# Performance work log

Hardware: AMD Instinct MI355X
Metric: run time of the kernel (lower is better)

## Reference

```python
import jax, jax.numpy as jnp
import numpy as np

DIM = 384
HEADS = 6
HIDDEN = int(DIM * 4.0)
EPS = 1e-6

def setup_inputs() -> dict:
    key = jax.random.key(0)
    ks = jax.random.split(key, 8)
    s = 0.02
    return {
        "x": jax.random.normal(ks[0], (4, 2048, DIM), dtype=jnp.float32),
        "w_qkv": jax.random.normal(ks[1], (DIM, 3 * DIM), dtype=jnp.float32) * s,
        "b_qkv": jnp.zeros((3 * DIM,), dtype=jnp.float32),
        "w_proj": jax.random.normal(ks[2], (DIM, DIM), dtype=jnp.float32) * s,
        "b_proj": jnp.zeros((DIM,), dtype=jnp.float32),
        "w_fc1": jax.random.normal(ks[3], (DIM, HIDDEN), dtype=jnp.float32) * s,
        "b_fc1": jnp.zeros((HIDDEN,), dtype=jnp.float32),
        "w_fc2": jax.random.normal(ks[4], (HIDDEN, DIM), dtype=jnp.float32) * s,
        "b_fc2": jnp.zeros((DIM,), dtype=jnp.float32),
        "g1": jnp.ones((DIM,), dtype=jnp.float32),
        "beta1": jnp.zeros((DIM,), dtype=jnp.float32),
        "g2": jnp.ones((DIM,), dtype=jnp.float32),
        "beta2": jnp.zeros((DIM,), dtype=jnp.float32),
    }

def _layernorm(x, g, b):
    mu = jnp.mean(x, axis=-1, keepdims=True)
    var = jnp.mean(jnp.square(x - mu), axis=-1, keepdims=True)
    return (x - mu) * jax.lax.rsqrt(var + EPS) * g + b

def _attention(x, w_qkv, b_qkv, w_proj, b_proj):
    B, N, C = x.shape
    H = HEADS
    Dh = C // H
    qkv = x @ w_qkv + b_qkv                      # [B,N,3C]
    qkv = qkv.reshape(B, N, 3, H, Dh)
    q = jnp.transpose(qkv[:, :, 0], (0, 2, 1, 3))  # [B,H,N,Dh]
    k = jnp.transpose(qkv[:, :, 1], (0, 2, 1, 3))
    v = jnp.transpose(qkv[:, :, 2], (0, 2, 1, 3))
    scale = Dh ** -0.5
    attn = jnp.einsum('bhnd,bhmd->bhnm', q, k) * scale
    attn = jax.nn.softmax(attn, axis=-1)
    out = jnp.einsum('bhnm,bhmd->bhnd', attn, v)
    out = jnp.transpose(out, (0, 2, 1, 3)).reshape(B, N, C)
    return out @ w_proj + b_proj

def _mlp(x, w_fc1, b_fc1, w_fc2, b_fc2):
    h = jax.nn.gelu(x @ w_fc1 + b_fc1, approximate=False)
    return h @ w_fc2 + b_fc2

def reference(x, w_qkv, b_qkv, w_proj, b_proj, w_fc1, b_fc1, w_fc2, b_fc2, g1, beta1, g2, beta2):
    x = x + _attention(_layernorm(x, g1, beta1), w_qkv, b_qkv, w_proj, b_proj)
    x = x + _mlp(_layernorm(x, g2, beta2), w_fc1, b_fc1, w_fc2, b_fc2)
    return x
```

## Files before the change

kernel.cpp:

```cpp
#include <hip/hip_runtime.h>
#include <hip/hip_bf16.h>

#define TOK 8192
#define CDIM 384
#define HEADS 6
#define DH 64
#define HID 1536
#define SEQ 2048

typedef short bf16x8 __attribute__((ext_vector_type(8)));
typedef float f32x4 __attribute__((ext_vector_type(4)));
typedef void __attribute__((address_space(1))) GV;
typedef void __attribute__((address_space(3))) SV;

__device__ __forceinline__ short f2bf(float f) {
    __hip_bfloat16 h = __float2bfloat16(f);
    return *reinterpret_cast<short*>(&h);
}

__device__ __forceinline__ int pack_bf2(float a, float b) {
    __hip_bfloat162 h2 = __float22bfloat162_rn(make_float2(a, b));
    int r;
    __builtin_memcpy(&r, &h2, 4);
    return r;
}

__device__ __forceinline__ void gl_lds16(const short* g, short* lds) {
    __builtin_amdgcn_global_load_lds((GV*)g, (SV*)lds, 16, 0, 0);
}

__device__ __forceinline__ float gelu_exact(float v) {
    return 0.5f * v * (1.0f + erff(v * 0.70710678118654752f));
}

#define SWZ4(r) ((((r) & 3) ^ (((r) >> 2) & 3)))

__global__ __launch_bounds__(128) void ln_kernel(const float* __restrict__ x,
                                                 const float* __restrict__ g,
                                                 const float* __restrict__ bta,
                                                 short* __restrict__ y) {
    const int row = blockIdx.x;
    const float* xr = x + (size_t)row * CDIM;
    const int t = threadIdx.x;
    float v0 = xr[t], v1 = xr[t + 128], v2 = xr[t + 256];
    float s = v0 + v1 + v2;
    float ss = v0 * v0 + v1 * v1 + v2 * v2;
#pragma unroll
    for (int off = 1; off < 64; off <<= 1) {
        s += __shfl_xor(s, off);
        ss += __shfl_xor(ss, off);
    }
    __shared__ float sh[4];
    const int wv = t >> 6;
    if ((t & 63) == 0) { sh[wv] = s; sh[2 + wv] = ss; }
    __syncthreads();
    s = sh[0] + sh[1];
    ss = sh[2] + sh[3];
    const float mu = s * (1.0f / CDIM);
    const float var = ss * (1.0f / CDIM) - mu * mu;
    const float rs = rsqrtf(var + 1e-6f);
    short* yr = y + (size_t)row * CDIM;
    yr[t]       = f2bf((v0 - mu) * rs * g[t]       + bta[t]);
    yr[t + 128] = f2bf((v1 - mu) * rs * g[t + 128] + bta[t + 128]);
    yr[t + 256] = f2bf((v2 - mu) * rs * g[t + 256] + bta[t + 256]);
}

__global__ __launch_bounds__(256) void transpose_bf16(const float* __restrict__ w,
                                                      short* __restrict__ wT,
                                                      int K, int N) {
    __shared__ float t[32][33];
    const int bx = blockIdx.x * 32, by = blockIdx.y * 32;
    const int tx = threadIdx.x & 31, ty = threadIdx.x >> 5;
#pragma unroll
    for (int i = 0; i < 4; ++i)
        t[ty + i * 8][tx] = w[(size_t)(by + ty + i * 8) * N + bx + tx];
    __syncthreads();
#pragma unroll
    for (int i = 0; i < 4; ++i)
        wT[(size_t)(bx + ty + i * 8) * K + by + tx] = f2bf(t[tx][ty + i * 8]);
}

template <int MODE, int MT>
__global__ __launch_bounds__(256) void mfma_gemm(const short* __restrict__ A,
                                                 const short* __restrict__ WT,
                                                 const float* __restrict__ bias,
                                                 const float* __restrict__ resid,
                                                 float* __restrict__ outF,
                                                 short* __restrict__ outB,
                                                 short* __restrict__ qb,
                                                 short* __restrict__ kb,
                                                 short* __restrict__ vtb,
                                                 int M, int N, int K) {
    constexpr int BN = (MT == 4) ? 128 : 64;
    __shared__ __align__(16) short As[128 * 32];
    __shared__ __align__(16) short Bs[BN * 32];

    const int tid  = threadIdx.x;
    const int w    = tid >> 6;
    const int lane = tid & 63;
    const int quad = lane >> 4;
    const int n15  = lane & 15;
    const int wr   = (MT == 4) ? (w >> 1) : w;
    const int wc   = (MT == 4) ? (w & 1) : 0;
    const int m0   = blockIdx.y * 128;
    const int n0   = blockIdx.x * BN;

    f32x4 acc[MT][4];
#pragma unroll
    for (int i = 0; i < MT; ++i)
#pragma unroll
        for (int j = 0; j < 4; ++j) {
            acc[i][j][0] = 0; acc[i][j][1] = 0; acc[i][j][2] = 0; acc[i][j][3] = 0;
        }

    const int ca0 = tid, ca1 = tid + 256;
    const int swz = SWZ4(n15);

    for (int k0 = 0; k0 < K; k0 += 32) {
        __syncthreads();
        gl_lds16(A  + (size_t)(m0 + (ca0 >> 2)) * K + k0 + (((ca0 & 3) ^ SWZ4(ca0 >> 2)) * 8), As + w * 512);
        gl_lds16(A  + (size_t)(m0 + (ca1 >> 2)) * K + k0 + (((ca1 & 3) ^ SWZ4(ca1 >> 2)) * 8), As + 2048 + w * 512);
        gl_lds16(WT + (size_t)(n0 + (ca0 >> 2)) * K + k0 + (((ca0 & 3) ^ SWZ4(ca0 >> 2)) * 8), Bs + w * 512);
        if (MT == 4)
            gl_lds16(WT + (size_t)(n0 + (ca1 >> 2)) * K + k0 + (((ca1 & 3) ^ SWZ4(ca1 >> 2)) * 8), Bs + 2048 + w * 512);
        __syncthreads();

        bf16x8 af[MT], bfr[4];
#pragma unroll
        for (int mt = 0; mt < MT; ++mt)
            af[mt] = *(const bf16x8*)&As[(wr * (MT * 16) + mt * 16 + n15) * 32 + ((quad ^ swz) * 8)];
#pragma unroll
        for (int nt = 0; nt < 4; ++nt)
            bfr[nt] = *(const bf16x8*)&Bs[(wc * 64 + nt * 16 + n15) * 32 + ((quad ^ swz) * 8)];
#pragma unroll
        for (int mt = 0; mt < MT; ++mt)
#pragma unroll
            for (int nt = 0; nt < 4; ++nt)
                acc[mt][nt] = __builtin_amdgcn_mfma_f32_16x16x32_bf16(af[mt], bfr[nt], acc[mt][nt], 0, 0, 0);
    }

#pragma unroll
    for (int nt = 0; nt < 4; ++nt) {
        const int col = n0 + wc * 64 + nt * 16 + n15;
        const float bv = bias[col];
        if constexpr (MODE == 2) {
            const int part = col / CDIM;
            const int rem  = col - part * CDIM;
            const int h    = rem >> 6;
            const int d    = rem & 63;
#pragma unroll
            for (int mt = 0; mt < MT; ++mt)
#pragma unroll
                for (int rr = 0; rr < 4; ++rr) {
                    const int r  = m0 + wr * (MT * 16) + mt * 16 + quad * 4 + rr;
                    const int bi = r >> 11;
                    const int n  = r & 2047;
                    float o = acc[mt][nt][rr] + bv;
                    if (part == 0) o *= 0.125f;
                    const short v = f2bf(o);
                    if (part == 0)
                        qb[((size_t)(bi * HEADS + h) * SEQ + n) * DH + d] = v;
                    else if (part == 1)
                        kb[((size_t)(bi * HEADS + h) * SEQ + n) * DH + d] = v;
                    else
                        vtb[((size_t)(bi * HEADS + h) * DH + d) * SEQ + n] = v;
                }
        } else {
#pragma unroll
            for (int mt = 0; mt < MT; ++mt)
#pragma unroll
                for (int rr = 0; rr < 4; ++rr) {
                    const int r = m0 + wr * (MT * 16) + mt * 16 + quad * 4 + rr;
                    float o = acc[mt][nt][rr] + bv;
                    if constexpr (MODE == 1) {
                        outB[(size_t)r * N + col] = f2bf(gelu_exact(o));
                    } else {
                        if (resid) o += resid[(size_t)r * N + col];
                        outF[(size_t)r * N + col] = o;
                    }
                }
        }
    }
}

__global__ __launch_bounds__(256) void attn_mfma(const short* __restrict__ qb,
                                                 const short* __restrict__ kb,
                                                 const short* __restrict__ vtb,
                                                 short* __restrict__ outp) {
    __shared__ __align__(16) short Ql[64 * 64];
    __shared__ __align__(16) short Kl[64 * 64];
    __shared__ __align__(16) short Vtl[64 * 64];

    const int qt = blockIdx.x;
    const int h  = blockIdx.y;
    const int b  = blockIdx.z;
    const int bh = b * HEADS + h;

    const int tid  = threadIdx.x;
    const int w    = tid >> 6;
    const int lane = tid & 63;
    const int quad = lane >> 4;
    const int n15  = lane & 15;
    const int swz  = n15 & 7;

    const size_t headoff = (size_t)bh * SEQ * DH;

    {
        const short* qg = qb + headoff + (size_t)qt * 64 * DH;
#pragma unroll
        for (int i = 0; i < 2; ++i) {
            const int c = (w * 2 + i) * 64 + lane;
            const int r = c >> 3, p = c & 7;
            gl_lds16(qg + r * 64 + ((p ^ (r & 7)) * 8), Ql + c * 8 - lane * 8 + lane * 8);
        }
    }

    f32x4 O[4];
    float m = -1e30f, l = 0.0f;
#pragma unroll
    for (int nt = 0; nt < 4; ++nt) { O[nt][0] = 0; O[nt][1] = 0; O[nt][2] = 0; O[nt][3] = 0; }

    bf16x8 qf[2];

    for (int kt = 0; kt < SEQ / 64; ++kt) {
        __syncthreads();
        {
            const short* kg = kb + headoff + (size_t)kt * 64 * DH;
#pragma unroll
            for (int i = 0; i < 2; ++i) {
                const int c = (w * 2 + i) * 64 + lane;
                const int r = c >> 3, p = c & 7;
                gl_lds16(kg + r * 64 + ((p ^ (r & 7)) * 8), Kl + (c - lane) * 8);
            }
            const short* vg0 = vtb + (size_t)bh * DH * SEQ + kt * 64;
#pragma unroll
            for (int i = 0; i < 2; ++i) {
                const int c = (w * 2 + i) * 64 + lane;
                const int r = c >> 3, p = c & 7;
                gl_lds16(vg0 + (size_t)r * SEQ + ((p ^ (r & 7)) * 8), Vtl + (c - lane) * 8);
            }
        }
        __syncthreads();

        if (kt == 0) {
            qf[0] = *(const bf16x8*)&Ql[(w * 16 + n15) * 64 + ((quad ^ swz) * 8)];
            qf[1] = *(const bf16x8*)&Ql[(w * 16 + n15) * 64 + (((4 + quad) ^ swz) * 8)];
        }

        f32x4 S[4];
#pragma unroll
        for (int nt = 0; nt < 4; ++nt) {
            S[nt][0] = 0; S[nt][1] = 0; S[nt][2] = 0; S[nt][3] = 0;
#pragma unroll
            for (int kc = 0; kc < 2; ++kc) {
                const bf16x8 kf = *(const bf16x8*)&Kl[(nt * 16 + n15) * 64 + (((kc * 4 + quad) ^ swz) * 8)];
                S[nt] = __builtin_amdgcn_mfma_f32_16x16x32_bf16(kf, qf[kc], S[nt], 0, 0, 0);
            }
        }

        float rm = S[0][0];
#pragma unroll
        for (int nt = 0; nt < 4; ++nt)
#pragma unroll
            for (int r = 0; r < 4; ++r)
                rm = fmaxf(rm, S[nt][r]);
        rm = fmaxf(rm, __shfl_xor(rm, 16));
        rm = fmaxf(rm, __shfl_xor(rm, 32));

        const float mn = fmaxf(m, rm);
        const float alpha = __expf(m - mn);
        m = mn;

        float rs = 0.0f;
        float sc[4][4];
#pragma unroll
        for (int nt = 0; nt < 4; ++nt)
#pragma unroll
            for (int r = 0; r < 4; ++r) {
                const float p = __expf(S[nt][r] - mn);
                sc[nt][r] = p;
                rs += p;
            }
        rs += __shfl_xor(rs, 16);
        rs += __shfl_xor(rs, 32);
        l = l * alpha + rs;

#pragma unroll
        for (int rr = 0; rr < 4; ++rr) {
            const float aO = __shfl(alpha, quad * 4 + rr);
#pragma unroll
            for (int nt = 0; nt < 4; ++nt)
                O[nt][rr] *= aO;
        }

        int pk01[4], pk23[4];
#pragma unroll
        for (int nt = 0; nt < 4; ++nt) {
            pk01[nt] = pack_bf2(sc[nt][0], sc[nt][1]);
            pk23[nt] = pack_bf2(sc[nt][2], sc[nt][3]);
        }

#pragma unroll
        for (int kc = 0; kc < 2; ++kc) {
            const int sel01 = (quad < 2) ? pk01[2 * kc] : pk01[2 * kc + 1];
            const int sel23 = (quad < 2) ? pk23[2 * kc] : pk23[2 * kc + 1];
            const int src0 = (((2 * quad) & 3) << 4) + n15;
            const int src1 = (((2 * quad + 1) & 3) << 4) + n15;
            int aw[4];
            aw[0] = __shfl(sel01, src0);
            aw[1] = __shfl(sel23, src0);
            aw[2] = __shfl(sel01, src1);
            aw[3] = __shfl(sel23, src1);
            bf16x8 af;
            __builtin_memcpy(&af, aw, 16);
#pragma unroll
            for (int nt = 0; nt < 4; ++nt) {
                const bf16x8 vf = *(const bf16x8*)&Vtl[(nt * 16 + n15) * 64 + (((kc * 4 + quad) ^ swz) * 8)];
                O[nt] = __builtin_amdgcn_mfma_f32_16x16x32_bf16(af, vf, O[nt], 0, 0, 0);
            }
        }
    }

    const float invq = 1.0f / l;
#pragma unroll
    for (int rr = 0; rr < 4; ++rr) {
        const float inv = __shfl(invq, quad * 4 + rr);
        const int row = qt * 64 + w * 16 + quad * 4 + rr;
#pragma unroll
        for (int nt = 0; nt < 4; ++nt)
            outp[(size_t)(b * SEQ + row) * CDIM + h * DH + nt * 16 + n15] = f2bf(O[nt][rr] * inv);
    }
}

extern "C" void kernel_launch(void* const* d_in, const int* in_sizes, int n_in,
                              void* d_out, int out_size, void* d_ws, size_t ws_size,
                              hipStream_t stream) {
    const float* x      = (const float*)d_in[0];
    const float* w_qkv  = (const float*)d_in[1];
    const float* b_qkv  = (const float*)d_in[2];
    const float* w_proj = (const float*)d_in[3];
    const float* b_proj = (const float*)d_in[4];
    const float* w_fc1  = (const float*)d_in[5];
    const float* b_fc1  = (const float*)d_in[6];
    const float* w_fc2  = (const float*)d_in[7];
    const float* b_fc2  = (const float*)d_in[8];
    const float* g1     = (const float*)d_in[9];
    const float* beta1  = (const float*)d_in[10];
    const float* g2     = (const float*)d_in[11];
    const float* beta2  = (const float*)d_in[12];
    float* out = (float*)d_out;

    short* qkvT = (short*)d_ws;
    short* projT = qkvT + 1152 * 384;
    short* fc1T  = projT + 384 * 384;
    short* fc2T  = fc1T + 1536 * 384;
    short* y     = fc2T + 384 * 1536;
    short* qb    = y + (size_t)TOK * 384;
    short* kb    = qb + (size_t)TOK * 384;
    short* vtb   = kb + (size_t)TOK * 384;
    short* attn  = vtb + (size_t)TOK * 384;
    short* hbuf  = attn + (size_t)TOK * 384;

    transpose_bf16<<<dim3(1152 / 32, 384 / 32), 256, 0, stream>>>(w_qkv, qkvT, CDIM, 3 * CDIM);
    transpose_bf16<<<dim3(384 / 32, 384 / 32), 256, 0, stream>>>(w_proj, projT, CDIM, CDIM);
    transpose_bf16<<<dim3(1536 / 32, 384 / 32), 256, 0, stream>>>(w_fc1, fc1T, CDIM, HID);
    transpose_bf16<<<dim3(384 / 32, 1536 / 32), 256, 0, stream>>>(w_fc2, fc2T, HID, CDIM);

    ln_kernel<<<TOK, 128, 0, stream>>>(x, g1, beta1, y);
    mfma_gemm<2, 4><<<dim3(1152 / 128, TOK / 128), 256, 0, stream>>>(
        y, qkvT, b_qkv, nullptr, nullptr, nullptr, qb, kb, vtb, TOK, 3 * CDIM, CDIM);
    attn_mfma<<<dim3(SEQ / 64, HEADS, 4), 256, 0, stream>>>(qb, kb, vtb, attn);
    mfma_gemm<0, 2><<<dim3(CDIM / 64, TOK / 128), 256, 0, stream>>>(
        attn, projT, b_proj, x, out, nullptr, nullptr, nullptr, nullptr, TOK, CDIM, CDIM);
    ln_kernel<<<TOK, 128, 0, stream>>>(out, g2, beta2, y);
    mfma_gemm<1, 4><<<dim3(HID / 128, TOK / 128), 256, 0, stream>>>(
        y, fc1T, b_fc1, nullptr, nullptr, hbuf, nullptr, nullptr, nullptr, TOK, HID, CDIM);
    mfma_gemm<0, 2><<<dim3(CDIM / 64, TOK / 128), 256, 0, stream>>>(
        hbuf, fc2T, b_fc2, out, out, nullptr, nullptr, nullptr, nullptr, TOK, CDIM, HID);
}
```

Baseline: 278.6 us.

## Double attention KV tile to 128 keys, use exp2 with folded log2e scale

The flash-attention kernel now processes 128 keys per iteration instead of 64, which halves the number of barrier pairs and online-softmax rescales per query tile. It precomputes the global load pointers for K and V once and advances them each step. The Q scale now includes log2(e), so the kernel can use exp2f instead of __expf. In exchange, LDS use and register pressure go up (8 score tiles per wave), which may lower occupancy.

```diff
diff --git a/kernel.cpp b/kernel.cpp
--- a/kernel.cpp
+++ b/kernel.cpp
@@ -7,6 +7,8 @@
 #define DH 64
 #define HID 1536
 #define SEQ 2048
+
+#define QSCALE 0.18033688011112042f
 
 typedef short bf16x8 __attribute__((ext_vector_type(8)));
 typedef float f32x4 __attribute__((ext_vector_type(4)));
@@ -156,7 +158,7 @@
                     const int bi = r >> 11;
                     const int n  = r & 2047;
                     float o = acc[mt][nt][rr] + bv;
-                    if (part == 0) o *= 0.125f;
+                    if (part == 0) o *= QSCALE;
                     const short v = f2bf(o);
                     if (part == 0)
                         qb[((size_t)(bi * HEADS + h) * SEQ + n) * DH + d] = v;
@@ -188,13 +190,11 @@
                                                  const short* __restrict__ vtb,
                                                  short* __restrict__ outp) {
     __shared__ __align__(16) short Ql[64 * 64];
-    __shared__ __align__(16) short Kl[64 * 64];
-    __shared__ __align__(16) short Vtl[64 * 64];
+    __shared__ __align__(16) short Kl[128 * 64];
+    __shared__ __align__(16) short Vtl[64 * 128];
 
     const int qt = blockIdx.x;
-    const int h  = blockIdx.y;
-    const int b  = blockIdx.z;
-    const int bh = b * HEADS + h;
+    const int bh = blockIdx.z * HEADS + blockIdx.y;
 
     const int tid  = threadIdx.x;
     const int w    = tid >> 6;
@@ -211,7 +211,22 @@
         for (int i = 0; i < 2; ++i) {
             const int c = (w * 2 + i) * 64 + lane;
             const int r = c >> 3, p = c & 7;
-            gl_lds16(qg + r * 64 + ((p ^ (r & 7)) * 8), Ql + c * 8 - lane * 8 + lane * 8);
+            gl_lds16(qg + r * 64 + ((p ^ (r & 7)) * 8), Ql + (c - lane) * 8);
+        }
+    }
+
+    const short* kptr[4];
+    const short* vptr[4];
+#pragma unroll
+    for (int i = 0; i < 4; ++i) {
+        const int c = (w * 4 + i) * 64 + lane;
+        {
+            const int r = c >> 3, p = c & 7;
+            kptr[i] = kb + headoff + r * 64 + ((p ^ (r & 7)) * 8);
+        }
+        {
+            const int r = c >> 4, p = c & 15;
+            vptr[i] = vtb + (size_t)bh * DH * SEQ + (size_t)r * SEQ + ((p ^ (r & 15)) * 8);
         }
     }
 
@@ -222,23 +237,14 @@
 
     bf16x8 qf[2];
 
-    for (int kt = 0; kt < SEQ / 64; ++kt) {
+    for (int kt = 0; kt < SEQ / 128; ++kt) {
         __syncthreads();
-        {
-            const short* kg = kb + headoff + (size_t)kt * 64 * DH;
-#pragma unroll
-            for (int i = 0; i < 2; ++i) {
-                const int c = (w * 2 + i) * 64 + lane;
-                const int r = c >> 3, p = c & 7;
-                gl_lds16(kg + r * 64 + ((p ^ (r & 7)) * 8), Kl + (c - lane) * 8);
-            }
-            const short* vg0 = vtb + (size_t)bh * DH * SEQ + kt * 64;
-#pragma unroll
-            for (int i = 0; i < 2; ++i) {
-                const int c = (w * 2 + i) * 64 + lane;
-                const int r = c >> 3, p = c & 7;
-                gl_lds16(vg0 + (size_t)r * SEQ + ((p ^ (r & 7)) * 8), Vtl + (c - lane) * 8);
-            }
+#pragma unroll
+        for (int i = 0; i < 4; ++i) {
+            gl_lds16(kptr[i], Kl + (w * 4 + i) * 512);
+            gl_lds16(vptr[i], Vtl + (w * 4 + i) * 512);
+            kptr[i] += 128 * DH;
+            vptr[i] += 128;
         }
         __syncthreads();
 
@@ -247,9 +253,9 @@
             qf[1] = *(const bf16x8*)&Ql[(w * 16 + n15) * 64 + (((4 + quad) ^ swz) * 8)];
         }
 
-        f32x4 S[4];
-#pragma unroll
-        for (int nt = 0; nt < 4; ++nt) {
+        f32x4 S[8];
+#pragma unroll
+        for (int nt = 0; nt < 8; ++nt) {
             S[nt][0] = 0; S[nt][1] = 0; S[nt][2] = 0; S[nt][3] = 0;
 #pragma unroll
             for (int kc = 0; kc < 2; ++kc) {
@@ -260,7 +266,7 @@
 
         float rm = S[0][0];
 #pragma unroll
-        for (int nt = 0; nt < 4; ++nt)
+        for (int nt = 0; nt < 8; ++nt)
 #pragma unroll
             for (int r = 0; r < 4; ++r)
                 rm = fmaxf(rm, S[nt][r]);
@@ -268,17 +274,16 @@
         rm = fmaxf(rm, __shfl_xor(rm, 32));
 
         const float mn = fmaxf(m, rm);
-        const float alpha = __expf(m - mn);
+        const float alpha = exp2f(m - mn);
         m = mn;
 
         float rs = 0.0f;
-        float sc[4][4];
-#pragma unroll
-        for (int nt = 0; nt < 4; ++nt)
+#pragma unroll
+        for (int nt = 0; nt < 8; ++nt)
 #pragma unroll
             for (int r = 0; r < 4; ++r) {
-                const float p = __expf(S[nt][r] - mn);
-                sc[nt][r] = p;
+                const float p = exp2f(S[nt][r] - mn);
+                S[nt][r] = p;
                 rs += p;
             }
         rs += __shfl_xor(rs, 16);
@@ -293,29 +298,40 @@
                 O[nt][rr] *= aO;
         }
 
-        int pk01[4], pk23[4];
-#pragma unroll
-        for (int nt = 0; nt < 4; ++nt) {
-            pk01[nt] = pack_bf2(sc[nt][0], sc[nt][1]);
-            pk23[nt] = pack_bf2(sc[nt][2], sc[nt][3]);
-        }
-
-#pragma unroll
-        for (int kc = 0; kc < 2; ++kc) {
-            const int sel01 = (quad < 2) ? pk01[2 * kc] : pk01[2 * kc + 1];
-            const int sel23 = (quad < 2) ? pk23[2 * kc] : pk23[2 * kc + 1];
-            const int src0 = (((2 * quad) & 3) << 4) + n15;
-            const int src1 = (((2 * quad + 1) & 3) << 4) + n15;
+        int pk01[8], pk23[8];
+#pragma unroll
+        for (int nt = 0; nt < 8; ++nt) {
+            pk01[nt] = pack_bf2(S[nt][0], S[nt][1]);
+            pk23[nt] = pack_bf2(S[nt][2], S[nt][3]);
+        }
+
+        const int src0 = ((quad & 1) * 2) * 16 + n15;
+        const int src1 = src0 + 16;
+        const bool hi = quad >= 2;
+#pragma unroll
+        for (int kc = 0; kc < 4; ++kc) {
             int aw[4];
-            aw[0] = __shfl(sel01, src0);
-            aw[1] = __shfl(sel23, src0);
-            aw[2] = __shfl(sel01, src1);
-            aw[3] = __shfl(sel23, src1);
+            {
+                const int lo0 = __shfl(pk01[2 * kc], src0), hi0 = __shfl(pk01[2 * kc + 1], src0);
+                aw[0] = hi ? hi0 : lo0;
+            }
+            {
+                const int lo1 = __shfl(pk23[2 * kc], src0), hi1 = __shfl(pk23[2 * kc + 1], src0);
+                aw[1] = hi ? hi1 : lo1;
+            }
+            {
+                const int lo2 = __shfl(pk01[2 * kc], src1), hi2 = __shfl(pk01[2 * kc + 1], src1);
+                aw[2] = hi ? hi2 : lo2;
+            }
+            {
+                const int lo3 = __shfl(pk23[2 * kc], src1), hi3 = __shfl(pk23[2 * kc + 1], src1);
+                aw[3] = hi ? hi3 : lo3;
+            }
             bf16x8 af;
             __builtin_memcpy(&af, aw, 16);
 #pragma unroll
             for (int nt = 0; nt < 4; ++nt) {
-                const bf16x8 vf = *(const bf16x8*)&Vtl[(nt * 16 + n15) * 64 + (((kc * 4 + quad) ^ swz) * 8)];
+                const bf16x8 vf = *(const bf16x8*)&Vtl[(nt * 16 + n15) * 128 + (((kc * 4 + quad) ^ n15) * 8)];
                 O[nt] = __builtin_amdgcn_mfma_f32_16x16x32_bf16(af, vf, O[nt], 0, 0, 0);
             }
         }
@@ -328,7 +344,8 @@
         const int row = qt * 64 + w * 16 + quad * 4 + rr;
 #pragma unroll
         for (int nt = 0; nt < 4; ++nt)
-            outp[(size_t)(b * SEQ + row) * CDIM + h * DH + nt * 16 + n15] = f2bf(O[nt][rr] * inv);
+            outp[(size_t)(blockIdx.z * SEQ + row) * CDIM + blockIdx.y * DH + nt * 16 + n15] =
+                f2bf(O[nt][rr] * inv);
     }
 }
 
```

After: 284.7 us. +2.2%, slower.
